# Optimization experiments

Hardware: AMD Instinct MI355X
Metric: run time of the kernel (lower is better)

Reference implementation:

```python
import jax, jax.numpy as jnp
import numpy as np

N_NODES = 100000


def gcn_conv(x, edge_index, W, b):
    """PyG GCNConv: add self-loops, symmetric deg^-1/2 normalization, linear."""
    n = x.shape[0]
    h = x @ W  # [N, out]
    loop = jnp.arange(n, dtype=edge_index.dtype)
    src = jnp.concatenate([edge_index[0], loop])
    dst = jnp.concatenate([edge_index[1], loop])
    deg = jax.ops.segment_sum(jnp.ones_like(dst, dtype=h.dtype), dst, num_segments=n)
    dinv = jnp.where(deg > 0, jax.lax.rsqrt(deg), 0.0)
    norm = dinv[src] * dinv[dst]  # [E+N]
    msg = h[src] * norm[:, None]  # gather + scale
    out = jax.ops.segment_sum(msg, dst, num_segments=n)  # scatter-add
    return out + b


def setup_inputs() -> dict:
    key = jax.random.key(0)
    k1, k2, k3, k4 = jax.random.split(key, 4)
    d_in, d_hid, d_out = 128, 128, 128  # output_dim // 2 = 128
    E = 1600000
    x = jax.random.normal(k1, (N_NODES, d_in), dtype=jnp.float32)
    edge_index = jax.random.randint(k2, (2, E), 0, N_NODES, dtype=jnp.int64)
    s1 = 1.0 / np.sqrt(d_in)
    s2 = 1.0 / np.sqrt(d_hid)
    W1 = jax.random.normal(k3, (d_in, d_hid), dtype=jnp.float32) * s1
    b1 = jnp.zeros((d_hid,), dtype=jnp.float32)
    W2 = jax.random.normal(k4, (d_hid, d_out), dtype=jnp.float32) * s2
    b2 = jnp.zeros((d_out,), dtype=jnp.float32)
    return {"x": x, "edge_index": edge_index, "W1": W1, "b1": b1, "W2": W2, "b2": b2}


def reference(x, edge_index, W1, b1, W2, b2):
    h = jax.nn.relu(gcn_conv(x, edge_index, W1, b1))
    # dropout(p=0.5) is identity in eval mode
    return gcn_conv(h, edge_index, W2, b2)
```

## Files before the change

kernel.cpp:

```cpp
#include <hip/hip_runtime.h>

#define D 128

typedef unsigned int uint;
typedef unsigned short ushort;
typedef __attribute__((ext_vector_type(8))) short bf16x8_t;
typedef __attribute__((ext_vector_type(4))) float f32x4_t;

#define BSH 9
#define BMASK 511
#define BN 512
#define CAP 9216
#define CHUNK 2048
#define NBUCKP 256

__device__ inline uint bf16rn(float f) {
    uint u = __float_as_uint(f);
    return (u + 0x7fffu + ((u >> 16) & 1u)) >> 16;
}

__global__ __launch_bounds__(256) void kp_scatter3(const int* __restrict__ src,
                                                   const int* __restrict__ dst,
                                                   int* __restrict__ gcnt,
                                                   uint* __restrict__ bkt, int E, int nbuck) {
    __shared__ uint stage[CHUNK];
    __shared__ int cnt[NBUCKP], loc[NBUCKP], gbase[NBUCKP];
    int t = threadIdx.x;
    int base = blockIdx.x * CHUNK;
    int end = min(E, base + CHUNK);

    cnt[t] = 0; gbase[t] = 0;
    __syncthreads();
    uint pk[8]; int bk[8]; int rk[8];
#pragma unroll
    for (int it = 0; it < 8; it++) {
        int i = base + t + it * 256;
        if (i < end) {
            int d = dst[i], s = src[i];
            bk[it] = d >> BSH;
            pk[it] = ((uint)s << BSH) | (uint)(d & BMASK);
            rk[it] = atomicAdd(&cnt[bk[it]], 1);
        } else {
            bk[it] = 0; pk[it] = 0u; rk[it] = -1;
        }
    }
    __syncthreads();
    int v = cnt[t];
    loc[t] = v;
    __syncthreads();
    for (int off = 1; off < NBUCKP; off <<= 1) {
        int x = (t >= off) ? loc[t - off] : 0;
        __syncthreads();
        loc[t] += x;
        __syncthreads();
    }
    if (t < nbuck && cnt[t] > 0)
        gbase[t] = atomicAdd(&gcnt[t], cnt[t]);
    __syncthreads();
#pragma unroll
    for (int it = 0; it < 8; it++)
        if (rk[it] >= 0)
            stage[(loc[bk[it]] - cnt[bk[it]]) + rk[it]] = pk[it];
    __syncthreads();
    int grp = t >> 4, gl = t & 15;
    for (int b2 = grp; b2 < nbuck; b2 += 16) {
        int c = cnt[b2];
        if (c == 0) continue;
        int lo = loc[b2] - c;
        int gb = gbase[b2];
        uint* ob = bkt + (size_t)b2 * CAP;
        for (int j = gl; j < c; j += 16) {
            int di = gb + j;
            if (di < CAP) ob[di] = stage[lo + j];
        }
    }
}

__global__ __launch_bounds__(512) void kp_build3(uint* __restrict__ bkt,
                                                 const int* __restrict__ gcnt,
                                                 int2* __restrict__ row_se,
                                                 float* __restrict__ dinv, int n, int nbuck,
                                                 const float* __restrict__ W1,
                                                 const float* __restrict__ W2,
                                                 ushort* __restrict__ W1h, ushort* __restrict__ W1l,
                                                 ushort* __restrict__ W2h, ushort* __restrict__ W2l) {
    int t = threadIdx.x, b = blockIdx.x;
    if (b >= nbuck) {
        int i = (b - nbuck) * 512 + t;
        int sel = i >> 14;
        int j = i & 16383;
        int k = j >> 7, nn = j & 127;
        const float* W = sel ? W2 : W1;
        float w = W[k * D + nn];
        uint hb = bf16rn(w);
        float hf = __uint_as_float(hb << 16);
        uint lb = bf16rn(w - hf);
        if (sel) { W2h[nn * D + k] = (ushort)hb; W2l[nn * D + k] = (ushort)lb; }
        else     { W1h[nn * D + k] = (ushort)hb; W1l[nn * D + k] = (ushort)lb; }
        return;
    }
    __shared__ uint ents[CAP];
    __shared__ ushort ranks[CAP];
    __shared__ int cnt[BN], loc[BN];
    int m = gcnt[b];
    if (m > CAP) m = CAP;
    uint* bk = bkt + (size_t)b * CAP;
    for (int i = t; i < m; i += 512) ents[i] = bk[i];
    cnt[t] = 0;
    __syncthreads();
    for (int i = t; i < m; i += 512) {
        int r = atomicAdd(&cnt[ents[i] & BMASK], 1);
        ranks[i] = (ushort)r;
    }
    __syncthreads();
    int v = cnt[t];
    loc[t] = v;
    __syncthreads();
    for (int off = 1; off < BN; off <<= 1) {
        int x = (t >= off) ? loc[t - off] : 0;
        __syncthreads();
        loc[t] += x;
        __syncthreads();
    }
    int base = b * CAP;
    int node = (b << BSH) + t;
    if (node < n) {
        row_se[node] = make_int2(base + loc[t] - v, base + loc[t]);
        dinv[node] = rsqrtf((float)(v + 1));
    }
    __syncthreads();
    for (int i = t; i < m; i += 512) {
        uint p = ents[i];
        int low = p & BMASK;
        ((int*)bk)[(loc[low] - cnt[low]) + (int)ranks[i]] = (int)((p >> BSH) << 8);
    }
}

__device__ inline void accum_bf16x8(float* a, uint4 v) {
    a[0] += __uint_as_float(v.x << 16);
    a[1] += __uint_as_float(v.x & 0xffff0000u);
    a[2] += __uint_as_float(v.y << 16);
    a[3] += __uint_as_float(v.y & 0xffff0000u);
    a[4] += __uint_as_float(v.z << 16);
    a[5] += __uint_as_float(v.z & 0xffff0000u);
    a[6] += __uint_as_float(v.w << 16);
    a[7] += __uint_as_float(v.w & 0xffff0000u);
}

__device__ inline void split8(float4 v0, float4 v1, bf16x8_t* hh, bf16x8_t* ll) {
    float f[8] = {v0.x, v0.y, v0.z, v0.w, v1.x, v1.y, v1.z, v1.w};
    bf16x8_t h, l;
#pragma unroll
    for (int i = 0; i < 8; i++) {
        uint hb = bf16rn(f[i]);
        float hf = __uint_as_float(hb << 16);
        uint lb = bf16rn(f[i] - hf);
        h[i] = (short)hb;
        l[i] = (short)lb;
    }
    *hh = h; *ll = l;
}

template <bool A_FP32>
__global__ __launch_bounds__(256, 2) void k_gemm_mfma(const void* __restrict__ A,
                                                      const ushort* __restrict__ Wth,
                                                      const ushort* __restrict__ Wtl,
                                                      const float* __restrict__ dinv,
                                                      ushort* __restrict__ Yb, int M) {
    constexpr int STR = 136;
    __shared__ ushort Wh[128 * STR];
    __shared__ ushort Wl[128 * STR];

    int t = threadIdx.x;
    int lane = t & 63, wave = t >> 6;
    int quad = lane >> 4, l16 = lane & 15;
    int m_off = (wave >> 1) * 64;
    int n_off = (wave & 1) * 64;
    int block_row = blockIdx.x * 128;

#pragma unroll
    for (int it = 0; it < 8; it++) {
        int s = t + it * 256;
        int nrow = s >> 4, kl = (s & 15) * 8;
        *(uint4*)&Wh[nrow * STR + kl] = *(const uint4*)(Wth + nrow * D + kl);
        *(uint4*)&Wl[nrow * STR + kl] = *(const uint4*)(Wtl + nrow * D + kl);
    }
    __syncthreads();

    f32x4_t acc[4][4];
#pragma unroll
    for (int mt = 0; mt < 4; mt++)
#pragma unroll
        for (int nt = 0; nt < 4; nt++) acc[mt][nt] = (f32x4_t){0.f, 0.f, 0.f, 0.f};

    const bf16x8_t zf = (bf16x8_t){0, 0, 0, 0, 0, 0, 0, 0};

#pragma unroll 2
    for (int ks = 0; ks < 4; ks++) {
        int kc = ks * 32 + quad * 8;
        bf16x8_t ah[4], al[4];
        if (A_FP32) {
            const float* Af = (const float*)A;
#pragma unroll
            for (int mt = 0; mt < 4; mt++) {
                int gr = block_row + m_off + mt * 16 + l16;
                float4 v0 = make_float4(0.f, 0.f, 0.f, 0.f);
                float4 v1 = make_float4(0.f, 0.f, 0.f, 0.f);
                if (gr < M) {
                    const float* rp = Af + (size_t)gr * D + kc;
                    v0 = *(const float4*)rp;
                    v1 = *(const float4*)(rp + 4);
                }
                split8(v0, v1, &ah[mt], &al[mt]);
            }
        } else {
            const ushort* Ab = (const ushort*)A;
#pragma unroll
            for (int mt = 0; mt < 4; mt++) {
                int gr = block_row + m_off + mt * 16 + l16;
                ah[mt] = (gr < M) ? *(const bf16x8_t*)(Ab + (size_t)gr * D + kc) : zf;
            }
        }
#pragma unroll
        for (int nt = 0; nt < 4; nt++) {
            bf16x8_t bh = *(const bf16x8_t*)&Wh[(n_off + nt * 16 + l16) * STR + kc];
            bf16x8_t bl = *(const bf16x8_t*)&Wl[(n_off + nt * 16 + l16) * STR + kc];
            if (A_FP32) {
#pragma unroll
                for (int mt = 0; mt < 4; mt++) {
                    acc[mt][nt] = __builtin_amdgcn_mfma_f32_16x16x32_bf16(ah[mt], bh, acc[mt][nt], 0, 0, 0);
                    acc[mt][nt] = __builtin_amdgcn_mfma_f32_16x16x32_bf16(al[mt], bh, acc[mt][nt], 0, 0, 0);
                    acc[mt][nt] = __builtin_amdgcn_mfma_f32_16x16x32_bf16(ah[mt], bl, acc[mt][nt], 0, 0, 0);
                }
            } else {
#pragma unroll
                for (int mt = 0; mt < 4; mt++) {
                    acc[mt][nt] = __builtin_amdgcn_mfma_f32_16x16x32_bf16(ah[mt], bh, acc[mt][nt], 0, 0, 0);
                    acc[mt][nt] = __builtin_amdgcn_mfma_f32_16x16x32_bf16(ah[mt], bl, acc[mt][nt], 0, 0, 0);
                }
            }
        }
    }

#pragma unroll
    for (int mt = 0; mt < 4; mt++) {
#pragma unroll
        for (int reg = 0; reg < 4; reg++) {
            int gr = block_row + m_off + mt * 16 + quad * 4 + reg;
            if (gr < M) {
                float di = dinv[gr];
#pragma unroll
                for (int nt = 0; nt < 4; nt++) {
                    int colg = n_off + nt * 16 + l16;
                    Yb[(size_t)gr * D + colg] = (ushort)bf16rn(di * acc[mt][nt][reg]);
                }
            }
        }
    }
}

__global__ __launch_bounds__(256) void k_agg(const ushort* __restrict__ Hb,
                                             const int2* __restrict__ row_se,
                                             const int* __restrict__ colb,
                                             const float* __restrict__ dinv,
                                             const float* __restrict__ bias,
                                             float* __restrict__ Yf, ushort* __restrict__ Yb,
                                             int n, int do_relu, int out_bf16) {
    __shared__ int ls[4][64];
    int wv = threadIdx.x >> 6;
    int node = blockIdx.x * 4 + wv;
    int lane = threadIdx.x & 63;
    int chain = lane >> 4;
    int l16   = lane & 15;
    if (node >= n) return;

    int2 se = row_se[node];
    int start = se.x, end = se.y;

    float a0[8], a1[8];
#pragma unroll
    for (int k = 0; k < 8; k++) { a0[k] = 0.f; a1[k] = 0.f; }

    const char* hbase = (const char*)Hb;
    uint loff = (uint)l16 * 16u;

    if (chain == 0) {
        uint4 v = *(const uint4*)(hbase + (uint)node * 256u + loff);
        accum_bf16x8(a0, v);
    }

    for (int tb = start; tb < end; tb += 64) {
        int idx = tb + lane;
        ls[wv][lane] = (idx < end) ? colb[idx] : 0;
        int c = min(64, end - tb);
        int j = chain;
        for (; j + 12 < c; j += 16) {
            uint o0 = (uint)ls[wv][j];
            uint o1 = (uint)ls[wv][j + 4];
            uint o2 = (uint)ls[wv][j + 8];
            uint o3 = (uint)ls[wv][j + 12];
            uint4 v0 = *(const uint4*)(hbase + o0 + loff);
            uint4 v1 = *(const uint4*)(hbase + o1 + loff);
            uint4 v2 = *(const uint4*)(hbase + o2 + loff);
            uint4 v3 = *(const uint4*)(hbase + o3 + loff);
            accum_bf16x8(a0, v0);
            accum_bf16x8(a1, v1);
            accum_bf16x8(a0, v2);
            accum_bf16x8(a1, v3);
        }
        for (; j + 4 < c; j += 8) {
            uint o0 = (uint)ls[wv][j];
            uint o1 = (uint)ls[wv][j + 4];
            uint4 v0 = *(const uint4*)(hbase + o0 + loff);
            uint4 v1 = *(const uint4*)(hbase + o1 + loff);
            accum_bf16x8(a0, v0);
            accum_bf16x8(a1, v1);
        }
        if (j < c) {
            uint o0 = (uint)ls[wv][j];
            uint4 v0 = *(const uint4*)(hbase + o0 + loff);
            accum_bf16x8(a0, v0);
        }
    }

    float acc[8];
#pragma unroll
    for (int k = 0; k < 8; k++) {
        float v = a0[k] + a1[k];
        v += __shfl_xor(v, 16, 64);
        v += __shfl_xor(v, 32, 64);
        acc[k] = v;
    }

    if (chain == 0) {
        float di = dinv[node];
        const float4* bp = (const float4*)bias + l16 * 2;
        float4 b0 = bp[0], b1 = bp[1];
        float o[8];
        o[0] = fmaf(di, acc[0], b0.x); o[1] = fmaf(di, acc[1], b0.y);
        o[2] = fmaf(di, acc[2], b0.z); o[3] = fmaf(di, acc[3], b0.w);
        o[4] = fmaf(di, acc[4], b1.x); o[5] = fmaf(di, acc[5], b1.y);
        o[6] = fmaf(di, acc[6], b1.z); o[7] = fmaf(di, acc[7], b1.w);
        if (do_relu) {
#pragma unroll
            for (int k = 0; k < 8; k++) o[k] = fmaxf(o[k], 0.f);
        }
        if (out_bf16) {
            uint4 pk;
            pk.x = bf16rn(o[0]) | (bf16rn(o[1]) << 16);
            pk.y = bf16rn(o[2]) | (bf16rn(o[3]) << 16);
            pk.z = bf16rn(o[4]) | (bf16rn(o[5]) << 16);
            pk.w = bf16rn(o[6]) | (bf16rn(o[7]) << 16);
            ((uint4*)(Yb + (size_t)node * D))[l16] = pk;
        } else {
            f32x4_t q0 = {o[0], o[1], o[2], o[3]};
            f32x4_t q1 = {o[4], o[5], o[6], o[7]};
            f32x4_t* yp = (f32x4_t*)(Yf + (size_t)node * D) + l16 * 2;
            __builtin_nontemporal_store(q0, yp);
            __builtin_nontemporal_store(q1, yp + 1);
        }
    }
}

extern "C" void kernel_launch(void* const* d_in, const int* in_sizes, int n_in,
                              void* d_out, int out_size, void* d_ws, size_t ws_size,
                              hipStream_t stream) {
    const float* x  = (const float*)d_in[0];
    const int*   ei = (const int*)d_in[1];
    const float* W1 = (const float*)d_in[2];
    const float* b1 = (const float*)d_in[3];
    const float* W2 = (const float*)d_in[4];
    const float* b2 = (const float*)d_in[5];
    float* out = (float*)d_out;

    int n = in_sizes[0] / D;
    int E = in_sizes[1] / 2;
    const int* src = ei;
    const int* dst = ei + E;

    int nbuck = (n + BMASK) >> BSH;

    char* p = (char*)d_ws;
    ushort* h_buf = (ushort*)p; p += (size_t)n * D * sizeof(ushort);
    ushort* y_buf = (ushort*)p; p += (size_t)n * D * sizeof(ushort);
    ushort* w1h   = (ushort*)p; p += (size_t)D * D * sizeof(ushort);
    ushort* w1l   = (ushort*)p; p += (size_t)D * D * sizeof(ushort);
    ushort* w2h   = (ushort*)p; p += (size_t)D * D * sizeof(ushort);
    ushort* w2l   = (ushort*)p; p += (size_t)D * D * sizeof(ushort);
    uint*  bkt    = (uint*)p;   p += (size_t)nbuck * CAP * sizeof(uint);
    float* dinv   = (float*)p;  p += (size_t)n * sizeof(float);
    int2*  row_se = (int2*)p;   p += (size_t)n * sizeof(int2);
    int*   gcnt   = (int*)p;    p += (size_t)nbuck * sizeof(int);

    (void)hipMemsetAsync(gcnt, 0, (size_t)nbuck * sizeof(int), stream);
    int sc_grid = (E + CHUNK - 1) / CHUNK;
    kp_scatter3<<<sc_grid, 256, 0, stream>>>(src, dst, gcnt, bkt, E, nbuck);
    kp_build3<<<nbuck + 64, 512, 0, stream>>>(bkt, gcnt, row_se, dinv, n, nbuck,
                                              W1, W2, w1h, w1l, w2h, w2l);

    int gemm_grid = (n + 127) / 128;
    int agg_grid  = (n + 3) / 4;
    const int* colp = (const int*)bkt;

    k_gemm_mfma<true><<<gemm_grid, 256, 0, stream>>>(x, w1h, w1l, dinv, h_buf, n);
    k_agg<<<agg_grid, 256, 0, stream>>>(h_buf, row_se, colp, dinv, b1, nullptr, y_buf, n, 1, 1);
    k_gemm_mfma<false><<<gemm_grid, 256, 0, stream>>>(y_buf, w2h, w2l, dinv, h_buf, n);
    k_agg<<<agg_grid, 256, 0, stream>>>(h_buf, row_se, colp, dinv, b2, out, nullptr, n, 0, 0);
}
```

Baseline: 314.2 us.

## Use wave-shuffle scans and 512-thread GEMM blocks with hoisted B fragments

Replaces the shared-memory Hillis-Steele prefix scans in the scatter and build kernels with wave-level shuffle scans plus a small cross-wave combine, removing many block barriers. The GEMM now uses 512-thread blocks covering 256 rows, so the weight tile copied into shared memory is reused across twice as many rows. Its inner loop is restructured to load B fragments once per k-step and stream A rows one at a time, which lowers register pressure. Launch bounds are raised to 512 threads with 4 blocks requested, which may force register spilling.

```diff
diff --git a/kernel.cpp b/kernel.cpp
--- a/kernel.cpp
+++ b/kernel.cpp
@@ -25,7 +25,9 @@
                                                    uint* __restrict__ bkt, int E, int nbuck) {
     __shared__ uint stage[CHUNK];
     __shared__ int cnt[NBUCKP], loc[NBUCKP], gbase[NBUCKP];
+    __shared__ int wtot[4];
     int t = threadIdx.x;
+    int lane = t & 63, w = t >> 6;
     int base = blockIdx.x * CHUNK;
     int end = min(E, base + CHUNK);
 
@@ -46,16 +48,21 @@
     }
     __syncthreads();
     int v = cnt[t];
-    loc[t] = v;
-    __syncthreads();
-    for (int off = 1; off < NBUCKP; off <<= 1) {
-        int x = (t >= off) ? loc[t - off] : 0;
-        __syncthreads();
-        loc[t] += x;
-        __syncthreads();
-    }
-    if (t < nbuck && cnt[t] > 0)
-        gbase[t] = atomicAdd(&gcnt[t], cnt[t]);
+    int sv = v;
+#pragma unroll
+    for (int off = 1; off < 64; off <<= 1) {
+        int x = __shfl_up(sv, off, 64);
+        sv += (lane >= off) ? x : 0;
+    }
+    if (lane == 63) wtot[w] = sv;
+    __syncthreads();
+    int add = 0;
+#pragma unroll
+    for (int i = 0; i < 4; i++) add += (i < w) ? wtot[i] : 0;
+    sv += add;
+    loc[t] = sv;
+    if (t < nbuck && v > 0)
+        gbase[t] = atomicAdd(&gcnt[t], v);
     __syncthreads();
 #pragma unroll
     for (int it = 0; it < 8; it++)
@@ -102,6 +109,8 @@
     __shared__ uint ents[CAP];
     __shared__ ushort ranks[CAP];
     __shared__ int cnt[BN], loc[BN];
+    __shared__ int wtot[8];
+    int lane = t & 63, w = t >> 6;
     int m = gcnt[b];
     if (m > CAP) m = CAP;
     uint* bk = bkt + (size_t)b * CAP;
@@ -114,18 +123,23 @@
     }
     __syncthreads();
     int v = cnt[t];
-    loc[t] = v;
-    __syncthreads();
-    for (int off = 1; off < BN; off <<= 1) {
-        int x = (t >= off) ? loc[t - off] : 0;
-        __syncthreads();
-        loc[t] += x;
-        __syncthreads();
-    }
+    int sv = v;
+#pragma unroll
+    for (int off = 1; off < 64; off <<= 1) {
+        int x = __shfl_up(sv, off, 64);
+        sv += (lane >= off) ? x : 0;
+    }
+    if (lane == 63) wtot[w] = sv;
+    __syncthreads();
+    int add = 0;
+#pragma unroll
+    for (int i = 0; i < 8; i++) add += (i < w) ? wtot[i] : 0;
+    sv += add;
+    loc[t] = sv;
     int base = b * CAP;
     int node = (b << BSH) + t;
     if (node < n) {
-        row_se[node] = make_int2(base + loc[t] - v, base + loc[t]);
+        row_se[node] = make_int2(base + sv - v, base + sv);
         dinv[node] = rsqrtf((float)(v + 1));
     }
     __syncthreads();
@@ -162,7 +176,7 @@
 }
 
 template <bool A_FP32>
-__global__ __launch_bounds__(256, 2) void k_gemm_mfma(const void* __restrict__ A,
+__global__ __launch_bounds__(512, 4) void k_gemm_mfma(const void* __restrict__ A,
                                                       const ushort* __restrict__ Wth,
                                                       const ushort* __restrict__ Wtl,
                                                       const float* __restrict__ dinv,
@@ -176,11 +190,11 @@
     int quad = lane >> 4, l16 = lane & 15;
     int m_off = (wave >> 1) * 64;
     int n_off = (wave & 1) * 64;
-    int block_row = blockIdx.x * 128;
-
-#pragma unroll
-    for (int it = 0; it < 8; it++) {
-        int s = t + it * 256;
+    int block_row = blockIdx.x * 256;
+
+#pragma unroll
+    for (int it = 0; it < 4; it++) {
+        int s = t + it * 512;
         int nrow = s >> 4, kl = (s & 15) * 8;
         *(uint4*)&Wh[nrow * STR + kl] = *(const uint4*)(Wth + nrow * D + kl);
         *(uint4*)&Wl[nrow * STR + kl] = *(const uint4*)(Wtl + nrow * D + kl);
@@ -195,15 +209,20 @@
 
     const bf16x8_t zf = (bf16x8_t){0, 0, 0, 0, 0, 0, 0, 0};
 
-#pragma unroll 2
     for (int ks = 0; ks < 4; ks++) {
         int kc = ks * 32 + quad * 8;
-        bf16x8_t ah[4], al[4];
-        if (A_FP32) {
-            const float* Af = (const float*)A;
-#pragma unroll
-            for (int mt = 0; mt < 4; mt++) {
-                int gr = block_row + m_off + mt * 16 + l16;
+        bf16x8_t bh[4], bl[4];
+#pragma unroll
+        for (int nt = 0; nt < 4; nt++) {
+            bh[nt] = *(const bf16x8_t*)&Wh[(n_off + nt * 16 + l16) * STR + kc];
+            bl[nt] = *(const bf16x8_t*)&Wl[(n_off + nt * 16 + l16) * STR + kc];
+        }
+#pragma unroll
+        for (int mt = 0; mt < 4; mt++) {
+            int gr = block_row + m_off + mt * 16 + l16;
+            bf16x8_t ah, al;
+            if (A_FP32) {
+                const float* Af = (const float*)A;
                 float4 v0 = make_float4(0.f, 0.f, 0.f, 0.f);
                 float4 v1 = make_float4(0.f, 0.f, 0.f, 0.f);
                 if (gr < M) {
@@ -211,32 +230,21 @@
                     v0 = *(const float4*)rp;
                     v1 = *(const float4*)(rp + 4);
                 }
-                split8(v0, v1, &ah[mt], &al[mt]);
+                split8(v0, v1, &ah, &al);
+            } else {
+                const ushort* Ab = (const ushort*)A;
+                ah = (gr < M) ? *(const bf16x8_t*)(Ab + (size_t)gr * D + kc) : zf;
+                al = zf;
             }
-        } else {
-            const ushort* Ab = (const ushort*)A;
-#pragma unroll
-            for (int mt = 0; mt < 4; mt++) {
-                int gr = block_row + m_off + mt * 16 + l16;
-                ah[mt] = (gr < M) ? *(const bf16x8_t*)(Ab + (size_t)gr * D + kc) : zf;
-            }
-        }
-#pragma unroll
-        for (int nt = 0; nt < 4; nt++) {
-            bf16x8_t bh = *(const bf16x8_t*)&Wh[(n_off + nt * 16 + l16) * STR + kc];
-            bf16x8_t bl = *(const bf16x8_t*)&Wl[(n_off + nt * 16 + l16) * STR + kc];
-            if (A_FP32) {
-#pragma unroll
-                for (int mt = 0; mt < 4; mt++) {
-                    acc[mt][nt] = __builtin_amdgcn_mfma_f32_16x16x32_bf16(ah[mt], bh, acc[mt][nt], 0, 0, 0);
-                    acc[mt][nt] = __builtin_amdgcn_mfma_f32_16x16x32_bf16(al[mt], bh, acc[mt][nt], 0, 0, 0);
-                    acc[mt][nt] = __builtin_amdgcn_mfma_f32_16x16x32_bf16(ah[mt], bl, acc[mt][nt], 0, 0, 0);
-                }
-            } else {
-#pragma unroll
-                for (int mt = 0; mt < 4; mt++) {
-                    acc[mt][nt] = __builtin_amdgcn_mfma_f32_16x16x32_bf16(ah[mt], bh, acc[mt][nt], 0, 0, 0);
-                    acc[mt][nt] = __builtin_amdgcn_mfma_f32_16x16x32_bf16(ah[mt], bl, acc[mt][nt], 0, 0, 0);
+#pragma unroll
+            for (int nt = 0; nt < 4; nt++) {
+                if (A_FP32) {
+                    acc[mt][nt] = __builtin_amdgcn_mfma_f32_16x16x32_bf16(ah, bh[nt], acc[mt][nt], 0, 0, 0);
+                    acc[mt][nt] = __builtin_amdgcn_mfma_f32_16x16x32_bf16(al, bh[nt], acc[mt][nt], 0, 0, 0);
+                    acc[mt][nt] = __builtin_amdgcn_mfma_f32_16x16x32_bf16(ah, bl[nt], acc[mt][nt], 0, 0, 0);
+                } else {
+                    acc[mt][nt] = __builtin_amdgcn_mfma_f32_16x16x32_bf16(ah, bh[nt], acc[mt][nt], 0, 0, 0);
+                    acc[mt][nt] = __builtin_amdgcn_mfma_f32_16x16x32_bf16(ah, bl[nt], acc[mt][nt], 0, 0, 0);
                 }
             }
         }
@@ -398,12 +406,12 @@
     kp_build3<<<nbuck + 64, 512, 0, stream>>>(bkt, gcnt, row_se, dinv, n, nbuck,
                                               W1, W2, w1h, w1l, w2h, w2l);
 
-    int gemm_grid = (n + 127) / 128;
+    int gemm_grid = (n + 255) / 256;
     int agg_grid  = (n + 3) / 4;
     const int* colp = (const int*)bkt;
 
-    k_gemm_mfma<true><<<gemm_grid, 256, 0, stream>>>(x, w1h, w1l, dinv, h_buf, n);
+    k_gemm_mfma<true><<<gemm_grid, 512, 0, stream>>>(x, w1h, w1l, dinv, h_buf, n);
     k_agg<<<agg_grid, 256, 0, stream>>>(h_buf, row_se, colp, dinv, b1, nullptr, y_buf, n, 1, 1);
-    k_gemm_mfma<false><<<gemm_grid, 256, 0, stream>>>(y_buf, w2h, w2l, dinv, h_buf, n);
+    k_gemm_mfma<false><<<gemm_grid, 512, 0, stream>>>(y_buf, w2h, w2l, dinv, h_buf, n);
     k_agg<<<agg_grid, 256, 0, stream>>>(h_buf, row_se, colp, dinv, b2, out, nullptr, n, 0, 0);
 }
```

After: 319.7 us. No clear change (+1.8%).
